# Kernel optimization log

Measured on AMD Instinct MI355X. Metric: run time of the kernel, lower is better.

Reference implementation:

```python
import jax, jax.numpy as jnp
import numpy as np

N_HEAD = 16
N_EMBD = 1024
SEQ = 2048
BATCH = 4


def setup_inputs() -> dict:
    key = jax.random.key(0)
    ks = jax.random.split(key, 5)
    s_in = 1.0 / np.sqrt(N_EMBD)
    return {
        "x": jax.random.normal(ks[0], (BATCH, SEQ, N_EMBD), dtype=jnp.float32),
        "W_attn": jax.random.normal(ks[1], (N_EMBD, 3 * N_EMBD), dtype=jnp.float32) * s_in,
        "b_attn": jax.random.normal(ks[2], (3 * N_EMBD,), dtype=jnp.float32) * 0.01,
        "W_proj": jax.random.normal(ks[3], (N_EMBD, N_EMBD), dtype=jnp.float32) * s_in,
        "b_proj": jax.random.normal(ks[4], (N_EMBD,), dtype=jnp.float32) * 0.01,
    }


def reference(x, W_attn, b_attn, W_proj, b_proj):
    B, T, C = x.shape
    H = N_HEAD
    D = C // H  # head dim
    qkv = x @ W_attn + b_attn                      # [B,T,3C]
    q, k, v = jnp.split(qkv, 3, axis=-1)
    # [B,T,C] -> [B,H,T,D]
    q = q.reshape(B, T, H, D).transpose(0, 2, 1, 3)
    k = k.reshape(B, T, H, D).transpose(0, 2, 1, 3)
    v = v.reshape(B, T, H, D).transpose(0, 2, 1, 3)
    scale = 1.0 / np.sqrt(D).astype(np.float32)
    att = jnp.einsum('bhqd,bhkd->bhqk', q, k) * scale   # [B,H,T,T]
    causal = jnp.tril(jnp.ones((T, T), dtype=bool))
    att = jnp.where(causal, att, jnp.finfo(att.dtype).min)
    att = jax.nn.softmax(att, axis=-1)
    y = jnp.einsum('bhqk,bhkd->bhqd', att, v)            # [B,H,T,D]
    y = y.transpose(0, 2, 1, 3).reshape(B, T, C)
    return y @ W_proj + b_proj
```

## Files before the change

### kernel.cpp

```cpp
#include <hip/hip_runtime.h>
#include <stdint.h>

typedef __attribute__((ext_vector_type(8))) short short8;
typedef __attribute__((ext_vector_type(4))) short short4v;
typedef __attribute__((ext_vector_type(4))) float f32x4;
typedef __attribute__((ext_vector_type(2))) unsigned int uint2v;

#define B_ 4
#define T_ 2048
#define C_ 1024
#define H_ 16
#define D_ 64
#define C3_ 3072

#define AS1 __attribute__((address_space(1)))
#define AS3 __attribute__((address_space(3)))

#define QK_SCALE 0.18033688f

__device__ __forceinline__ unsigned short f2bf(float f) {
    union { float f; uint32_t u; } v; v.f = f;
    uint32_t r = v.u + 0x7FFFu + ((v.u >> 16) & 1u);
    return (unsigned short)(r >> 16);
}

__device__ __forceinline__ uint32_t pk_bf16(float lo, float hi) {
    uint32_t r;
    asm("v_cvt_pk_bf16_f32 %0, %1, %2" : "=v"(r) : "v"(lo), "v"(hi));
    return r;
}

__global__ void k_cvt_bf16(const float* __restrict__ in, unsigned short* __restrict__ out, int n4) {
    int i = blockIdx.x * blockDim.x + threadIdx.x;
    if (i >= n4) return;
    float4 v = ((const float4*)in)[i];
    unsigned short o0 = f2bf(v.x), o1 = f2bf(v.y), o2 = f2bf(v.z), o3 = f2bf(v.w);
    unsigned long long packed = (unsigned long long)o0 | ((unsigned long long)o1 << 16)
        | ((unsigned long long)o2 << 32) | ((unsigned long long)o3 << 48);
    *(unsigned long long*)(out + (size_t)i * 4) = packed;
}

__global__ void k_wtrans(const float* __restrict__ W, unsigned short* __restrict__ WT, int K, int N) {
    __shared__ float t[32][33];
    int n0 = blockIdx.x * 32, k0 = blockIdx.y * 32;
    int tx = threadIdx.x, ty = threadIdx.y;
#pragma unroll
    for (int i = 0; i < 4; ++i)
        t[ty + i * 8][tx] = W[(size_t)(k0 + ty + i * 8) * N + n0 + tx];
    __syncthreads();
#pragma unroll
    for (int i = 0; i < 4; ++i)
        WT[(size_t)(n0 + ty + i * 8) * K + k0 + tx] = f2bf(t[tx][ty + i * 8]);
}

__global__ void k_prep_vt(const unsigned short* __restrict__ qkv, unsigned short* __restrict__ vt) {
    int bh = blockIdx.y; int b = bh >> 4, h = bh & 15;
    int t0 = blockIdx.x * 64;
    __shared__ unsigned short tile[64][72];
    int tid = threadIdx.x;
    int r = tid >> 3;
    int c = (tid & 7) * 8;
#pragma unroll
    for (int rr = 0; rr < 64; rr += 32) {
        const unsigned short* src = qkv + (size_t)(b * T_ + t0 + r + rr) * C3_ + 2 * C_ + h * D_ + c;
        short8 v = *(const short8*)src;
#pragma unroll
        for (int j = 0; j < 8; ++j) tile[r + rr][c + j] = (unsigned short)v[j];
    }
    __syncthreads();
#pragma unroll
    for (int rr = 0; rr < 64; rr += 32) {
        int d = r + rr;
        short8 sv;
#pragma unroll
        for (int j = 0; j < 8; ++j) sv[j] = (short)tile[c + j][d];
        *(short8*)(vt + (size_t)bh * D_ * T_ + (size_t)d * T_ + t0 + c) = sv;
    }
}

template<bool OUT_BF16>
__global__ __launch_bounds__(256, 2) void k_gemm_bt(const unsigned short* __restrict__ A,
                                                    const unsigned short* __restrict__ BT,
                                                    const float* __restrict__ bias,
                                                    unsigned short* __restrict__ outb,
                                                    float* __restrict__ outf,
                                                    int M, int N, int K) {
    __shared__ __align__(16) char arena[73728];
    int tid = threadIdx.x;
    int w = tid >> 6, lane = tid & 63;
    int wrow = w >> 1, wcol = w & 1;

    int lin = blockIdx.y * gridDim.x + blockIdx.x;
    int nwg8 = (gridDim.x * gridDim.y) >> 3;
    int newlin = (lin & 7) * nwg8 + (lin >> 3);
    int bx = newlin % gridDim.x;
    int by = newlin / gridDim.x;
    int m0 = by * 256, n0 = bx * 128;

    int lr = lane & 15, lg = lane >> 4;

    f32x4 acc[8][4] = {};

    int grow = tid >> 2;
    int scb = ((tid & 3) << 4) ^ (((tid >> 3) & 3) << 4);
    const char* sA[4];
    const char* sB[2];
#pragma unroll
    for (int rr = 0; rr < 4; ++rr)
        sA[rr] = (const char*)A + (size_t)(m0 + grow + rr * 64) * K * 2 + scb;
#pragma unroll
    for (int rr = 0; rr < 2; ++rr)
        sB[rr] = (const char*)BT + (size_t)(n0 + grow + rr * 64) * K * 2 + scb;

    int inner = (lg * 16) ^ (((lr >> 1) & 3) << 4);
    int aoff = wrow * 8192 + lr * 64 + inner;
    int boff = 16384 + wcol * 4096 + lr * 64 + inner;

#define GSTAGE(OFS)                                                                                 \
    {                                                                                               \
        _Pragma("unroll")                                                                           \
        for (int rr = 0; rr < 4; ++rr) {                                                            \
            __builtin_amdgcn_global_load_lds((const AS1 void*)sA[rr],                               \
                (AS3 void*)(arena + (OFS) + tid * 16 + rr * 4096), 16, 0, 0);                       \
            sA[rr] += 64;                                                                           \
        }                                                                                           \
        _Pragma("unroll")                                                                           \
        for (int rr = 0; rr < 2; ++rr) {                                                            \
            __builtin_amdgcn_global_load_lds((const AS1 void*)sB[rr],                               \
                (AS3 void*)(arena + (OFS) + 16384 + tid * 16 + rr * 4096), 16, 0, 0);               \
            sB[rr] += 64;                                                                           \
        }                                                                                           \
    }

#define GCOMPUTE(OFS)                                                                               \
    {                                                                                               \
        short8 af[8], bf[4];                                                                        \
        _Pragma("unroll")                                                                           \
        for (int i = 0; i < 8; ++i)                                                                 \
            af[i] = *(const short8*)(arena + (OFS) + aoff + i * 1024);                              \
        _Pragma("unroll")                                                                           \
        for (int j = 0; j < 4; ++j)                                                                 \
            bf[j] = *(const short8*)(arena + (OFS) + boff + j * 1024);                              \
        __builtin_amdgcn_s_setprio(1);                                                              \
        _Pragma("unroll")                                                                           \
        for (int i = 0; i < 8; ++i)                                                                 \
            _Pragma("unroll")                                                                       \
            for (int j = 0; j < 4; ++j)                                                             \
                acc[i][j] = __builtin_amdgcn_mfma_f32_16x16x32_bf16(af[i], bf[j], acc[i][j], 0, 0, 0); \
        __builtin_amdgcn_s_setprio(0);                                                              \
    }

    int NT = K >> 5;
    int ofs0 = 0, ofs1 = 24576, ofs2 = 49152;

    GSTAGE(ofs0);
    GSTAGE(ofs1);
    asm volatile("s_waitcnt vmcnt(6)" ::: "memory");
    __builtin_amdgcn_s_barrier();
    __builtin_amdgcn_sched_barrier(0);

    for (int t = 0; t < NT; ++t) {
        bool pf = (t + 2 < NT);
        if (pf) GSTAGE(ofs2);
        GCOMPUTE(ofs0);
        if (pf) { asm volatile("s_waitcnt vmcnt(6)" ::: "memory"); }
        else    { asm volatile("s_waitcnt vmcnt(0)" ::: "memory"); }
        __builtin_amdgcn_s_barrier();
        __builtin_amdgcn_sched_barrier(0);
        int tmp = ofs0; ofs0 = ofs1; ofs1 = ofs2; ofs2 = tmp;
    }
#undef GSTAGE
#undef GCOMPUTE

#pragma unroll
    for (int i = 0; i < 8; ++i) {
        int row = m0 + wrow * 128 + i * 16 + lg * 4;
#pragma unroll
        for (int j = 0; j < 4; ++j) {
            int col = n0 + wcol * 64 + j * 16 + lr;
            float bv = bias[col];
#pragma unroll
            for (int r = 0; r < 4; ++r) {
                float v = acc[i][j][r] + bv;
                if (OUT_BF16) {
                    if (col < C_) v *= QK_SCALE;
                    outb[(size_t)(row + r) * N + col] = f2bf(v);
                } else {
                    outf[(size_t)(row + r) * N + col] = v;
                }
            }
        }
    }
}

__global__ __launch_bounds__(256, 4) void k_attn(const unsigned short* __restrict__ qkv,
                                                 const unsigned short* __restrict__ vt,
                                                 unsigned short* __restrict__ y) {
    __shared__ __align__(16) char arena[40960];
    int tid = threadIdx.x;
    int w = tid >> 6, lane = tid & 63;
    int lr = lane & 15, lg = lane >> 4;

    int bid = blockIdx.x;
    int bid2 = (bid & 7) * 128 + (bid >> 3);
    int bh = bid2 >> 4, pair = bid2 & 15;
    int b = bh >> 4, h = bh & 15;

    const unsigned short* kbase = qkv + (size_t)(b * T_) * C3_ + C_ + h * D_;
    const unsigned short* vtb = vt + (size_t)bh * D_ * T_;

    int sw_ = (lr & 7) << 4;
    int RB0 = lr * 128 + ((lg * 16) ^ sw_);
    int RB1 = RB0 ^ 64;
    int jl = (lr >> 1) & 3;
    int pbase = 32768 + w * 2048 + lr * 128
              + ((((lg >> 1) ^ (lr & 1)) << 4) | (((lg & 1) ^ (lr >> 3)) << 3));
    int pwa[4];
#pragma unroll
    for (int j = 0; j < 4; ++j) pwa[j] = pbase + ((j ^ jl) << 5);
    int prd0 = 32768 + w * 2048 + lr * 128 + ((lg ^ (lr & 7)) << 4);
    int prd1 = prd0 ^ 64;
    int hs = lr & 8;
    int prA0a = prd0 + hs,       prA0b = prd0 + (8 ^ hs);
    int prA1a = prd1 + hs,       prA1b = prd1 + (8 ^ hs);

    int row0 = tid >> 3, row1 = 32 + (tid >> 3);
    int scol0 = ((tid & 7) << 4) ^ ((row0 & 7) << 4);
    int scol1 = ((tid & 7) << 4) ^ ((row1 & 7) << 4);

    const char *sK0, *sK1, *sV0, *sV1;

#define ASTAGE(LDSOFF)                                                                                  \
    {                                                                                                   \
        __builtin_amdgcn_global_load_lds((const AS1 void*)sK0, (AS3 void*)(arena + (LDSOFF) + w * 1024), 16, 0, 0);          \
        __builtin_amdgcn_global_load_lds((const AS1 void*)sK1, (AS3 void*)(arena + (LDSOFF) + 4096 + w * 1024), 16, 0, 0);   \
        __builtin_amdgcn_global_load_lds((const AS1 void*)sV0, (AS3 void*)(arena + 16384 + (LDSOFF) + w * 1024), 16, 0, 0);  \
        __builtin_amdgcn_global_load_lds((const AS1 void*)sV1, (AS3 void*)(arena + 16384 + (LDSOFF) + 4096 + w * 1024), 16, 0, 0); \
        sK0 += 64 * C3_ * 2; sK1 += 64 * C3_ * 2; sV0 += 128; sV1 += 128;                               \
    }

#define ACOMPUTE(LDSOFF, KT)                                                                            \
    {                                                                                                   \
        f32x4 s[4];                                                                                     \
        __builtin_amdgcn_s_setprio(1);                                                                  \
        _Pragma("unroll")                                                                               \
        for (int j = 0; j < 4; ++j) {                                                                   \
            short8 kf0 = *(const short8*)(arena + RB0 + (LDSOFF) + j * 2048);                           \
            short8 kf1 = *(const short8*)(arena + RB1 + (LDSOFF) + j * 2048);                           \
            f32x4 z = {};                                                                               \
            z = __builtin_amdgcn_mfma_f32_16x16x32_bf16(kf0, qf0, z, 0, 0, 0);                          \
            s[j] = __builtin_amdgcn_mfma_f32_16x16x32_bf16(kf1, qf1, z, 0, 0, 0);                       \
        }                                                                                               \
        __builtin_amdgcn_s_setprio(0);                                                                  \
        if ((KT) == ntiles - 1) {                                                                       \
            int kb = (KT) * 64 + lg * 4 - qv;                                                           \
            _Pragma("unroll")                                                                           \
            for (int j = 0; j < 4; ++j)                                                                 \
                _Pragma("unroll")                                                                       \
                for (int r = 0; r < 4; ++r)                                                             \
                    if (kb + j * 16 + r > 0) s[j][r] = -INFINITY;                                       \
        }                                                                                               \
        _Pragma("unroll")                                                                               \
        for (int j = 0; j < 4; ++j)                                                                     \
            _Pragma("unroll")                                                                           \
            for (int r = 0; r < 4; ++r) {                                                               \
                float pv = __builtin_amdgcn_exp2f(s[j][r]);                                             \
                s[j][r] = pv;                                                                           \
                ls += pv;                                                                               \
            }                                                                                           \
        _Pragma("unroll")                                                                               \
        for (int j = 0; j < 4; ++j) {                                                                   \
            uint2v W;                                                                                   \
            W[0] = pk_bf16(s[j][0], s[j][1]);                                                           \
            W[1] = pk_bf16(s[j][2], s[j][3]);                                                           \
            *(uint2v*)(arena + pwa[j]) = W;                                                             \
        }                                                                                               \
        short4v l0 = *(const short4v*)(arena + prA0a);                                                  \
        short4v h0 = *(const short4v*)(arena + prA0b);                                                  \
        short4v l1 = *(const short4v*)(arena + prA1a);                                                  \
        short4v h1 = *(const short4v*)(arena + prA1b);                                                  \
        short8 pa0 = __builtin_shufflevector(l0, h0, 0, 1, 2, 3, 4, 5, 6, 7);                           \
        short8 pa1 = __builtin_shufflevector(l1, h1, 0, 1, 2, 3, 4, 5, 6, 7);                           \
        __builtin_amdgcn_s_setprio(1);                                                                  \
        _Pragma("unroll")                                                                               \
        for (int dt = 0; dt < 4; ++dt) {                                                                \
            short8 vf0 = *(const short8*)(arena + RB0 + 16384 + (LDSOFF) + dt * 2048);                  \
            short8 vf1 = *(const short8*)(arena + RB1 + 16384 + (LDSOFF) + dt * 2048);                  \
            o[dt] = __builtin_amdgcn_mfma_f32_16x16x32_bf16(pa0, vf0, o[dt], 0, 0, 0);                  \
            o[dt] = __builtin_amdgcn_mfma_f32_16x16x32_bf16(pa1, vf1, o[dt], 0, 0, 0);                  \
        }                                                                                               \
        __builtin_amdgcn_s_setprio(0);                                                                  \
    }

#pragma unroll 1
    for (int half = 0; half < 2; ++half) {
        int qt = half ? (31 - pair) : pair;
        int q0 = qt * 64;
        int ntiles = qt + 1;

        const unsigned short* qrow = qkv + (size_t)(b * T_ + q0 + w * 16 + lr) * C3_ + h * D_;
        short8 qf0 = *(const short8*)(qrow + lg * 8);
        short8 qf1 = *(const short8*)(qrow + 32 + lg * 8);

        f32x4 o[4] = {};
        float ls = 0.f;
        int qv = q0 + w * 16 + lr;

        sK0 = (const char*)(kbase + (size_t)row0 * C3_) + scol0;
        sK1 = (const char*)(kbase + (size_t)row1 * C3_) + scol1;
        sV0 = (const char*)(vtb + (size_t)row0 * T_) + scol0;
        sV1 = (const char*)(vtb + (size_t)row1 * T_) + scol1;

        ASTAGE(0);
        asm volatile("s_waitcnt vmcnt(0)" ::: "memory");
        __syncthreads();

#pragma unroll 1
        for (int kt = 0; kt < ntiles; kt += 2) {
            if (kt + 1 < ntiles) ASTAGE(8192);
            ACOMPUTE(0, kt);
            asm volatile("s_waitcnt vmcnt(0)" ::: "memory");
            __syncthreads();
            if (kt + 1 < ntiles) {
                if (kt + 2 < ntiles) ASTAGE(0);
                ACOMPUTE(8192, kt + 1);
                asm volatile("s_waitcnt vmcnt(0)" ::: "memory");
                __syncthreads();
            }
        }

        ls += __shfl_xor(ls, 16);
        ls += __shfl_xor(ls, 32);
#pragma unroll
        for (int r = 0; r < 4; ++r) {
            float lst = __shfl(ls, lg * 4 + r, 64);
            float inv = 1.0f / lst;
            int q = q0 + w * 16 + lg * 4 + r;
            unsigned short* yrow = y + (size_t)(b * T_ + q) * C_ + h * D_;
#pragma unroll
            for (int dt = 0; dt < 4; ++dt)
                yrow[dt * 16 + lr] = f2bf(o[dt][r] * inv);
        }
    }
#undef ASTAGE
#undef ACOMPUTE
}

extern "C" void kernel_launch(void* const* d_in, const int* in_sizes, int n_in,
                              void* d_out, int out_size, void* d_ws, size_t ws_size,
                              hipStream_t stream) {
    const float* x  = (const float*)d_in[0];
    const float* Wa = (const float*)d_in[1];
    const float* ba = (const float*)d_in[2];
    const float* Wp = (const float*)d_in[3];
    const float* bp = (const float*)d_in[4];
    float* out = (float*)d_out;

    char* ws = (char*)d_ws;
    unsigned short* xb  = (unsigned short*)(ws);
    unsigned short* wat = (unsigned short*)(ws + 16777216);
    unsigned short* wpt = (unsigned short*)(ws + 23068672);
    unsigned short* qkv = (unsigned short*)(ws + 25165824);
    unsigned short* vt  = (unsigned short*)(ws + 75497472);
    unsigned short* y   = xb;

    k_cvt_bf16<<<8192, 256, 0, stream>>>(x, xb, (B_ * T_ * C_) / 4);
    k_wtrans<<<dim3(C3_ / 32, C_ / 32), dim3(32, 8), 0, stream>>>(Wa, wat, C_, C3_);
    k_wtrans<<<dim3(C_ / 32, C_ / 32), dim3(32, 8), 0, stream>>>(Wp, wpt, C_, C_);
    k_gemm_bt<true><<<dim3(C3_ / 128, (B_ * T_) / 256), 256, 0, stream>>>(
        xb, wat, ba, qkv, nullptr, B_ * T_, C3_, C_);
    k_prep_vt<<<dim3(T_ / 64, B_ * H_), 256, 0, stream>>>(qkv, vt);
    k_attn<<<1024, 256, 0, stream>>>(qkv, vt, y);
    k_gemm_bt<false><<<dim3(C_ / 128, (B_ * T_) / 256), 256, 0, stream>>>(
        y, wpt, bp, nullptr, out, B_ * T_, C_, C_);
}
```

Before: 159.9 us.

## Triple-buffer K/V tiles in attention kernel with prefetch two tiles ahead

Moves the attention K/V staging from a double buffer to a three-deep rotating LDS buffer, prefetching two tiles ahead. The wait drops from vmcnt(0) to vmcnt(4), so one tile's loads can stay in flight across the barrier. LDS use grows to 56KB and launch bounds drop to 2 blocks per SM, which lowers occupancy. The barrier is now a raw s_barrier plus sched_barrier, so correctness depends on the counted vmcnt waits.

```diff
diff --git a/kernel.cpp b/kernel.cpp
--- a/kernel.cpp
+++ b/kernel.cpp
@@ -193,10 +193,10 @@
     }
 }
 
-__global__ __launch_bounds__(256, 4) void k_attn(const unsigned short* __restrict__ qkv,
+__global__ __launch_bounds__(256, 2) void k_attn(const unsigned short* __restrict__ qkv,
                                                  const unsigned short* __restrict__ vt,
                                                  unsigned short* __restrict__ y) {
-    __shared__ __align__(16) char arena[40960];
+    __shared__ __align__(16) char arena[57344];
     int tid = threadIdx.x;
     int w = tid >> 6, lane = tid & 63;
     int lr = lane & 15, lg = lane >> 4;
@@ -213,12 +213,12 @@
     int RB0 = lr * 128 + ((lg * 16) ^ sw_);
     int RB1 = RB0 ^ 64;
     int jl = (lr >> 1) & 3;
-    int pbase = 32768 + w * 2048 + lr * 128
+    int pbase = 49152 + w * 2048 + lr * 128
               + ((((lg >> 1) ^ (lr & 1)) << 4) | (((lg & 1) ^ (lr >> 3)) << 3));
     int pwa[4];
 #pragma unroll
     for (int j = 0; j < 4; ++j) pwa[j] = pbase + ((j ^ jl) << 5);
-    int prd0 = 32768 + w * 2048 + lr * 128 + ((lg ^ (lr & 7)) << 4);
+    int prd0 = 49152 + w * 2048 + lr * 128 + ((lg ^ (lr & 7)) << 4);
     int prd1 = prd0 ^ 64;
     int hs = lr & 8;
     int prA0a = prd0 + hs,       prA0b = prd0 + (8 ^ hs);
@@ -230,23 +230,23 @@
 
     const char *sK0, *sK1, *sV0, *sV1;
 
-#define ASTAGE(LDSOFF)                                                                                  \
+#define ASTAGE(KOFS)                                                                                    \
     {                                                                                                   \
-        __builtin_amdgcn_global_load_lds((const AS1 void*)sK0, (AS3 void*)(arena + (LDSOFF) + w * 1024), 16, 0, 0);          \
-        __builtin_amdgcn_global_load_lds((const AS1 void*)sK1, (AS3 void*)(arena + (LDSOFF) + 4096 + w * 1024), 16, 0, 0);   \
-        __builtin_amdgcn_global_load_lds((const AS1 void*)sV0, (AS3 void*)(arena + 16384 + (LDSOFF) + w * 1024), 16, 0, 0);  \
-        __builtin_amdgcn_global_load_lds((const AS1 void*)sV1, (AS3 void*)(arena + 16384 + (LDSOFF) + 4096 + w * 1024), 16, 0, 0); \
+        __builtin_amdgcn_global_load_lds((const AS1 void*)sK0, (AS3 void*)(arena + (KOFS) + w * 1024), 16, 0, 0);            \
+        __builtin_amdgcn_global_load_lds((const AS1 void*)sK1, (AS3 void*)(arena + (KOFS) + 4096 + w * 1024), 16, 0, 0);     \
+        __builtin_amdgcn_global_load_lds((const AS1 void*)sV0, (AS3 void*)(arena + 24576 + (KOFS) + w * 1024), 16, 0, 0);    \
+        __builtin_amdgcn_global_load_lds((const AS1 void*)sV1, (AS3 void*)(arena + 24576 + (KOFS) + 4096 + w * 1024), 16, 0, 0); \
         sK0 += 64 * C3_ * 2; sK1 += 64 * C3_ * 2; sV0 += 128; sV1 += 128;                               \
     }
 
-#define ACOMPUTE(LDSOFF, KT)                                                                            \
+#define ACOMPUTE(KOFS, KT)                                                                              \
     {                                                                                                   \
         f32x4 s[4];                                                                                     \
         __builtin_amdgcn_s_setprio(1);                                                                  \
         _Pragma("unroll")                                                                               \
         for (int j = 0; j < 4; ++j) {                                                                   \
-            short8 kf0 = *(const short8*)(arena + RB0 + (LDSOFF) + j * 2048);                           \
-            short8 kf1 = *(const short8*)(arena + RB1 + (LDSOFF) + j * 2048);                           \
+            short8 kf0 = *(const short8*)(arena + RB0 + (KOFS) + j * 2048);                             \
+            short8 kf1 = *(const short8*)(arena + RB1 + (KOFS) + j * 2048);                             \
             f32x4 z = {};                                                                               \
             z = __builtin_amdgcn_mfma_f32_16x16x32_bf16(kf0, qf0, z, 0, 0, 0);                          \
             s[j] = __builtin_amdgcn_mfma_f32_16x16x32_bf16(kf1, qf1, z, 0, 0, 0);                       \
@@ -284,8 +284,8 @@
         __builtin_amdgcn_s_setprio(1);                                                                  \
         _Pragma("unroll")                                                                               \
         for (int dt = 0; dt < 4; ++dt) {                                                                \
-            short8 vf0 = *(const short8*)(arena + RB0 + 16384 + (LDSOFF) + dt * 2048);                  \
-            short8 vf1 = *(const short8*)(arena + RB1 + 16384 + (LDSOFF) + dt * 2048);                  \
+            short8 vf0 = *(const short8*)(arena + RB0 + 24576 + (KOFS) + dt * 2048);                    \
+            short8 vf1 = *(const short8*)(arena + RB1 + 24576 + (KOFS) + dt * 2048);                    \
             o[dt] = __builtin_amdgcn_mfma_f32_16x16x32_bf16(pa0, vf0, o[dt], 0, 0, 0);                  \
             o[dt] = __builtin_amdgcn_mfma_f32_16x16x32_bf16(pa1, vf1, o[dt], 0, 0, 0);                  \
         }                                                                                               \
@@ -311,22 +311,28 @@
         sV0 = (const char*)(vtb + (size_t)row0 * T_) + scol0;
         sV1 = (const char*)(vtb + (size_t)row1 * T_) + scol1;
 
-        ASTAGE(0);
-        asm volatile("s_waitcnt vmcnt(0)" ::: "memory");
-        __syncthreads();
+        int kofs0 = 0, kofs1 = 8192, kofs2 = 16384;
+
+        ASTAGE(kofs0);
+        if (ntiles > 1) {
+            ASTAGE(kofs1);
+            asm volatile("s_waitcnt vmcnt(4)" ::: "memory");
+        } else {
+            asm volatile("s_waitcnt vmcnt(0)" ::: "memory");
+        }
+        __builtin_amdgcn_s_barrier();
+        __builtin_amdgcn_sched_barrier(0);
 
 #pragma unroll 1
-        for (int kt = 0; kt < ntiles; kt += 2) {
-            if (kt + 1 < ntiles) ASTAGE(8192);
-            ACOMPUTE(0, kt);
-            asm volatile("s_waitcnt vmcnt(0)" ::: "memory");
-            __syncthreads();
-            if (kt + 1 < ntiles) {
-                if (kt + 2 < ntiles) ASTAGE(0);
-                ACOMPUTE(8192, kt + 1);
-                asm volatile("s_waitcnt vmcnt(0)" ::: "memory");
-                __syncthreads();
-            }
+        for (int kt = 0; kt < ntiles; ++kt) {
+            bool pf = (kt + 2 < ntiles);
+            if (pf) ASTAGE(kofs2);
+            ACOMPUTE(kofs0, kt);
+            if (pf) { asm volatile("s_waitcnt vmcnt(4)" ::: "memory"); }
+            else    { asm volatile("s_waitcnt vmcnt(0)" ::: "memory"); }
+            __builtin_amdgcn_s_barrier();
+            __builtin_amdgcn_sched_barrier(0);
+            int tmp = kofs0; kofs0 = kofs1; kofs1 = kofs2; kofs2 = tmp;
         }
 
         ls += __shfl_xor(ls, 16);
```

New measurement: 169.5 us. +6.0%, slower.
